# Kernel optimization log

Hardware: AMD Instinct MI355X
Metric: run time of the kernel (lower is better)

Reference implementation:

```python
import jax, jax.numpy as jnp
import numpy as np

D_MODEL = 1024
NUM_HEADS = 16
HEAD_DIM = D_MODEL // NUM_HEADS


def setup_inputs() -> dict:
    key = jax.random.key(0)
    ks = jax.random.split(key, 9)
    s = 1.0 / np.sqrt(D_MODEL)  # torch Linear default init range scale
    def lin(k):
        kw, kb = jax.random.split(k)
        W = jax.random.uniform(kw, (D_MODEL, D_MODEL), jnp.float32, -s, s)
        b = jax.random.uniform(kb, (D_MODEL,), jnp.float32, -s, s)
        return W, b
    Wq, bq = lin(ks[0])
    Wk, bk = lin(ks[1])
    Wv, bv = lin(ks[2])
    Wo, bo = lin(ks[3])
    x = jax.random.normal(ks[4], (4, 2048, D_MODEL), jnp.float32)
    return {"x": x, "Wq": Wq, "bq": bq, "Wk": Wk, "bk": bk,
            "Wv": Wv, "bv": bv, "Wo": Wo, "bo": bo}


def reference(x, Wq, bq, Wk, bk, Wv, bv, Wo, bo):
    B, S, _ = x.shape
    H, Dh = NUM_HEADS, HEAD_DIM
    scale = Dh ** -0.5
    # projections; W stored as [in, out] so y = x @ W + b
    q = (x @ Wq + bq).reshape(B, S, H, Dh).transpose(0, 2, 1, 3)  # [B,H,S,Dh]
    k = (x @ Wk + bk).reshape(B, S, H, Dh).transpose(0, 2, 1, 3)
    v = (x @ Wv + bv).reshape(B, S, H, Dh).transpose(0, 2, 1, 3)
    scores = jnp.einsum('bhqd,bhkd->bhqk', q, k) * scale  # [B,H,S,S]
    causal = jnp.tril(jnp.ones((S, S), dtype=bool))
    scores = jnp.where(causal[None, None], scores, jnp.finfo(scores.dtype).min)
    attn = jax.nn.softmax(scores, axis=-1)
    out = jnp.einsum('bhqk,bhkd->bhqd', attn, v)  # [B,H,S,Dh]
    out = out.transpose(0, 2, 1, 3).reshape(B, S, H * Dh)
    return out @ Wo + bo
```

## Files before the change

kernel.cpp:

```cpp
#include <hip/hip_runtime.h>
#include <math.h>

#define DM 1024
#define NH 16
#define DH 64
#define BB 4
#define SS 2048
#define MROWS (BB*SS)

typedef __bf16 bf16;
typedef __bf16 bf16x8 __attribute__((ext_vector_type(8)));
typedef float floatx4 __attribute__((ext_vector_type(4)));

#if __has_builtin(__builtin_amdgcn_exp2f)
#define EXP2F __builtin_amdgcn_exp2f
#else
#define EXP2F exp2f
#endif

#define QSCALE (0.125f * 1.44269504088896f)

__device__ __forceinline__ void cp16(void* lds, const void* g) {
  __builtin_amdgcn_global_load_lds(
      (__attribute__((address_space(1))) void*)(void*)g,
      (__attribute__((address_space(3))) void*)lds,
      16, 0, 0);
}

__global__ __launch_bounds__(256) void cvt_x(
    const float* __restrict__ X, bf16* __restrict__ Y) {
  int i = (blockIdx.x * 256 + threadIdx.x) * 8;
  float4 a = *(const float4*)&X[i];
  float4 b = *(const float4*)&X[i + 4];
  bf16x8 o;
  o[0] = (bf16)a.x; o[1] = (bf16)a.y; o[2] = (bf16)a.z; o[3] = (bf16)a.w;
  o[4] = (bf16)b.x; o[5] = (bf16)b.y; o[6] = (bf16)b.z; o[7] = (bf16)b.w;
  *(bf16x8*)&Y[i] = o;
}

__global__ __launch_bounds__(1024) void wtransc(
    const float* __restrict__ W0, const float* __restrict__ W1,
    const float* __restrict__ W2, const float* __restrict__ W3,
    bf16* __restrict__ T0, bf16* __restrict__ T1,
    bf16* __restrict__ T2, bf16* __restrict__ T3) {
  __shared__ float tile[32][33];
  const float* W; bf16* T;
  int z = blockIdx.z;
  if (z == 0)      { W = W0; T = T0; }
  else if (z == 1) { W = W1; T = T1; }
  else if (z == 2) { W = W2; T = T2; }
  else             { W = W3; T = T3; }
  int tx = threadIdx.x, ty = threadIdx.y;
  tile[ty][tx] = W[(blockIdx.y * 32 + ty) * DM + blockIdx.x * 32 + tx];
  __syncthreads();
  T[(blockIdx.x * 32 + ty) * DM + blockIdx.y * 32 + tx] = (bf16)tile[tx][ty];
}

#define BK 32
#define TST 136

__global__ __launch_bounds__(256, 3) void gemm_qkv(
    const bf16* __restrict__ A, const bf16* __restrict__ WT,
    const float* __restrict__ bq, const float* __restrict__ bk,
    const float* __restrict__ bv,
    bf16* __restrict__ qb, bf16* __restrict__ kb, bf16* __restrict__ vt) {
  __shared__ __align__(16) char smem[2 * 128 * BK * 2 * 2 > 128 * TST * 2
                                         ? 2 * 128 * BK * 2 * 2
                                         : 128 * TST * 2];
  bf16* As = (bf16*)smem;
  bf16* Bs = (bf16*)smem + 2 * 128 * BK;
  bf16* Ts = (bf16*)smem;

  int tid = threadIdx.x;
  int lane = tid & 63, w = tid >> 6;
  int wm = (w >> 1) * 64;
  int wn = (w & 1) * 64;
  int m0 = blockIdx.y * 128;
  int n0 = blockIdx.x * 128;
  int which = n0 >> 10;
  int qd = lane >> 4;
  int l15 = lane & 15;

  floatx4 acc[4][4] = {};

  auto stage = [&](int pb, int k0) {
    for (int i = 0; i < 2; ++i) {
      int ci = (w * 2 + i) * 64;
      int c = ci + lane;
      int r = c >> 2, cc = (c & 3) * 8;
      cp16(&As[pb * 128 * BK + ci * 8], &A[(size_t)(m0 + r) * DM + k0 + cc]);
      cp16(&Bs[pb * 128 * BK + ci * 8], &WT[(size_t)(n0 + r) * DM + k0 + cc]);
    }
  };

  stage(0, 0);
  __syncthreads();

  for (int t = 0; t < DM / BK; ++t) {
    int pb = t & 1;
    if (t + 1 < DM / BK) stage(pb ^ 1, (t + 1) * BK);
    bf16x8 af[4], bfr[4];
    for (int mt = 0; mt < 4; ++mt)
      af[mt] = *(const bf16x8*)&As[pb * 128 * BK + (wm + mt * 16 + l15) * BK + qd * 8];
    for (int nt = 0; nt < 4; ++nt)
      bfr[nt] = *(const bf16x8*)&Bs[pb * 128 * BK + (wn + nt * 16 + l15) * BK + qd * 8];
    for (int mt = 0; mt < 4; ++mt)
      for (int nt = 0; nt < 4; ++nt)
        acc[mt][nt] = __builtin_amdgcn_mfma_f32_16x16x32_bf16(
            af[mt], bfr[nt], acc[mt][nt], 0, 0, 0);
    __syncthreads();
  }

  const float* bias = (which == 0) ? bq : (which == 1) ? bk : bv;

  if (which == 2) {
    for (int nt = 0; nt < 4; ++nt) {
      int cl = wn + nt * 16 + l15;
      float bv_ = bias[(n0 & 1023) + cl];
      for (int mt = 0; mt < 4; ++mt)
        for (int r = 0; r < 4; ++r)
          Ts[cl * TST + wm + mt * 16 + qd * 4 + r] = (bf16)(acc[mt][nt][r] + bv_);
    }
    __syncthreads();
    int chunk = tid & 15, colb = tid >> 4;
    for (int p = 0; p < 8; ++p) {
      int cl = p * 16 + colb;
      bf16x8 vv = *(const bf16x8*)&Ts[cl * TST + chunk * 8];
      *(bf16x8*)&vt[(size_t)((n0 & 1023) + cl) * MROWS + m0 + chunk * 8] = vv;
    }
  } else {
    bf16* out = (which == 0) ? qb : kb;
    float sc = (which == 0) ? QSCALE : 1.0f;
    for (int nt = 0; nt < 4; ++nt) {
      int col = (n0 & 1023) + wn + nt * 16 + l15;
      float bv_ = bias[col];
      for (int mt = 0; mt < 4; ++mt)
        for (int r = 0; r < 4; ++r) {
          int row = m0 + wm + mt * 16 + qd * 4 + r;
          out[(size_t)row * DM + col] = (bf16)((acc[mt][nt][r] + bv_) * sc);
        }
    }
  }
}

__global__ __launch_bounds__(256, 4) void gemm_out(
    const bf16* __restrict__ A, const bf16* __restrict__ WT,
    const float* __restrict__ bias, float* __restrict__ C) {
  __shared__ __align__(16) bf16 As[2][64 * BK];
  __shared__ __align__(16) bf16 Bs[2][128 * BK];
  int tid = threadIdx.x;
  int lane = tid & 63, w = tid >> 6;
  int wm = (w >> 1) * 32;
  int wn = (w & 1) * 64;
  int m0 = blockIdx.x * 64;
  int n0 = blockIdx.y * 128;
  int qd = lane >> 4;
  int l15 = lane & 15;

  floatx4 acc[2][4] = {};

  auto stage = [&](int pb, int k0) {
    {
      int ci = w * 64;
      int c = ci + lane;
      int r = c >> 2, cc = (c & 3) * 8;
      cp16(&As[pb][ci * 8], &A[(size_t)(m0 + r) * DM + k0 + cc]);
    }
    for (int i = 0; i < 2; ++i) {
      int ci = (w * 2 + i) * 64;
      int c = ci + lane;
      int r = c >> 2, cc = (c & 3) * 8;
      cp16(&Bs[pb][ci * 8], &WT[(size_t)(n0 + r) * DM + k0 + cc]);
    }
  };

  stage(0, 0);
  __syncthreads();

  for (int t = 0; t < DM / BK; ++t) {
    int pb = t & 1;
    if (t + 1 < DM / BK) stage(pb ^ 1, (t + 1) * BK);
    bf16x8 af[2], bfr[4];
    for (int mt = 0; mt < 2; ++mt)
      af[mt] = *(const bf16x8*)&As[pb][(wm + mt * 16 + l15) * BK + qd * 8];
    for (int nt = 0; nt < 4; ++nt)
      bfr[nt] = *(const bf16x8*)&Bs[pb][(wn + nt * 16 + l15) * BK + qd * 8];
    for (int mt = 0; mt < 2; ++mt)
      for (int nt = 0; nt < 4; ++nt)
        acc[mt][nt] = __builtin_amdgcn_mfma_f32_16x16x32_bf16(
            af[mt], bfr[nt], acc[mt][nt], 0, 0, 0);
    __syncthreads();
  }

  for (int nt = 0; nt < 4; ++nt) {
    int col = n0 + wn + nt * 16 + l15;
    float bv = bias[col];
    for (int mt = 0; mt < 2; ++mt)
      for (int r = 0; r < 4; ++r) {
        int row = m0 + wm + mt * 16 + qd * 4 + r;
        C[(size_t)row * DM + col] = acc[mt][nt][r] + bv;
      }
  }
}

__global__ __launch_bounds__(512, 4) void attn_fwd(
    const bf16* __restrict__ Qg, const bf16* __restrict__ Kg,
    const bf16* __restrict__ Vt, bf16* __restrict__ O) {
  __shared__ __align__(16) bf16 Kbuf[2][64 * 64];
  __shared__ __align__(16) bf16 Vbuf[2][64 * 64];
  __shared__ __align__(16) bf16 Ps[8][16][72];

  int tid = threadIdx.x;
  int lane = tid & 63, w = tid >> 6;
  int qd = lane >> 4, l15 = lane & 15;
  int sw = l15 & 7;
  int pair = blockIdx.x, h = blockIdx.y, b = blockIdx.z;
  int base = b * SS;
  int hoff = h * DH;

  int gch = ((lane & 7) ^ (lane >> 3)) * 8;
  auto stage = [&](int pb, int kt) {
    int kbase = base + kt * 64;
    int ci = w * 64;
    int row = (ci + lane) >> 3;
    cp16(&Kbuf[pb][ci * 8], &Kg[(size_t)(kbase + row) * DM + hoff + gch]);
    cp16(&Vbuf[pb][ci * 8],
         &Vt[(size_t)(hoff + row) * MROWS + base + kt * 64 + gch]);
  };

  bf16x8 onesf;
  for (int j = 0; j < 8; ++j) onesf[j] = (bf16)1.0f;

  for (int ph = 0; ph < 2; ++ph) {
    int qt = ph ? (15 - pair) : pair;
    int q0 = qt * 128;
    int nkt = 2 * qt + 2;

    stage(0, 0);

    bf16x8 qf[2];
    {
      int qrow = base + q0 + w * 16 + l15;
      for (int ks = 0; ks < 2; ++ks)
        qf[ks] = *(const bf16x8*)&Qg[(size_t)qrow * DM + hoff + ks * 32 + qd * 8];
    }

    float m_r = -3e38f;
    floatx4 lacc = {};
    floatx4 oacc[4] = {};

    __syncthreads();

    for (int kt = 0; kt < nkt; ++kt) {
      int pb = kt & 1;
      if (kt + 1 < nkt) stage(pb ^ 1, kt + 1);

      floatx4 s[4] = {};
      for (int ks = 0; ks < 2; ++ks)
        for (int nt = 0; nt < 4; ++nt) {
          bf16x8 kf = *(const bf16x8*)
              &Kbuf[pb][(nt * 16 + l15) * 64 + (((ks << 2) + qd) ^ sw) * 8];
          s[nt] = __builtin_amdgcn_mfma_f32_16x16x32_bf16(
              qf[ks], kf, s[nt], 0, 0, 0);
        }

      if (kt >= 2 * qt) {
        for (int nt = 0; nt < 4; ++nt) {
          int col = kt * 64 + nt * 16 + l15;
          for (int r = 0; r < 4; ++r) {
            int row = q0 + w * 16 + qd * 4 + r;
            if (col > row) s[nt][r] = -3e38f;
          }
        }
      }

      {
        float t = s[0][0];
        for (int nt = 0; nt < 4; ++nt)
          for (int r = 0; r < 4; ++r) t = fmaxf(t, s[nt][r]);
        t = fmaxf(t, __shfl_xor(t, 1, 64));
        t = fmaxf(t, __shfl_xor(t, 2, 64));
        t = fmaxf(t, __shfl_xor(t, 4, 64));
        t = fmaxf(t, __shfl_xor(t, 8, 64));
        float mn = fmaxf(m_r, t);
        float al = EXP2F(m_r - mn);
        m_r = mn;
        for (int dt = 0; dt < 4; ++dt)
          for (int r = 0; r < 4; ++r) oacc[dt][r] *= al;
        for (int r = 0; r < 4; ++r) lacc[r] *= al;
        for (int nt = 0; nt < 4; ++nt)
          for (int r = 0; r < 4; ++r) {
            float p = EXP2F(s[nt][r] - mn);
            Ps[w][qd * 4 + r][nt * 16 + l15] = (bf16)p;
          }
      }

      bf16x8 pf[2];
      for (int ks = 0; ks < 2; ++ks)
        pf[ks] = *(const bf16x8*)&Ps[w][l15][ks * 32 + qd * 8];

      for (int ks = 0; ks < 2; ++ks)
        for (int dt = 0; dt < 4; ++dt) {
          bf16x8 vf = *(const bf16x8*)
              &Vbuf[pb][(dt * 16 + l15) * 64 + (((ks << 2) + qd) ^ sw) * 8];
          oacc[dt] = __builtin_amdgcn_mfma_f32_16x16x32_bf16(
              pf[ks], vf, oacc[dt], 0, 0, 0);
        }
      for (int ks = 0; ks < 2; ++ks)
        lacc = __builtin_amdgcn_mfma_f32_16x16x32_bf16(
            pf[ks], onesf, lacc, 0, 0, 0);

      __syncthreads();
    }

    for (int r = 0; r < 4; ++r) {
      float inv = 1.0f / lacc[r];
      int row = base + q0 + w * 16 + qd * 4 + r;
      for (int dt = 0; dt < 4; ++dt)
        O[(size_t)row * DM + hoff + dt * 16 + l15] = (bf16)(oacc[dt][r] * inv);
    }
  }
}

extern "C" void kernel_launch(void* const* d_in, const int* in_sizes, int n_in,
                              void* d_out, int out_size, void* d_ws, size_t ws_size,
                              hipStream_t stream) {
  const float* x  = (const float*)d_in[0];
  const float* Wq = (const float*)d_in[1];
  const float* bq = (const float*)d_in[2];
  const float* Wk = (const float*)d_in[3];
  const float* bk = (const float*)d_in[4];
  const float* Wv = (const float*)d_in[5];
  const float* bv = (const float*)d_in[6];
  const float* Wo = (const float*)d_in[7];
  const float* bo = (const float*)d_in[8];
  float* out = (float*)d_out;

  char* ws = (char*)d_ws;
  const size_t act = (size_t)MROWS * DM * sizeof(bf16);
  bf16* xb    = (bf16*)(ws);
  bf16* qb    = (bf16*)(ws + act);
  bf16* kb    = (bf16*)(ws + 2 * act);
  bf16* vt    = (bf16*)(ws + 3 * act);
  bf16* ab    = (bf16*)(ws + 4 * act);
  bf16* WqkvT = (bf16*)(ws + 5 * act);
  bf16* WoT   = WqkvT + 3 * (size_t)DM * DM;

  cvt_x<<<MROWS * DM / (256 * 8), 256, 0, stream>>>(x, xb);
  wtransc<<<dim3(32, 32, 4), dim3(32, 32), 0, stream>>>(
      Wq, Wk, Wv, Wo,
      WqkvT, WqkvT + (size_t)DM * DM, WqkvT + 2 * (size_t)DM * DM, WoT);

  gemm_qkv<<<dim3(24, 64), 256, 0, stream>>>(
      xb, WqkvT, bq, bk, bv, qb, kb, vt);

  attn_fwd<<<dim3(8, NH, BB), 512, 0, stream>>>(qb, kb, vt, ab);

  gemm_out<<<dim3(128, 8), 256, 0, stream>>>(ab, WoT, bo, out);
}
```

Measured before the change: 268.3 us.

## Keep attention probabilities in registers via transposed QK and permlane swaps

The QK^T MFMA now runs with swapped operands, so each lane holds scores for a single query row. Probabilities are packed to bf16 and rearranged into the PV operand layout with permlane32/16 swaps, which removes the LDS round trip through the Ps buffer. Row sums are accumulated in registers instead of through an extra MFMA against a ones vector. The online softmax also skips rescaling when the new max stays within a threshold of the running max, which cuts exp and multiply work but lets unnormalized values grow by up to 2^11.

```diff
diff --git a/kernel.cpp b/kernel.cpp
--- a/kernel.cpp
+++ b/kernel.cpp
@@ -9,8 +9,11 @@
 #define MROWS (BB*SS)
 
 typedef __bf16 bf16;
+typedef __bf16 bf16x2 __attribute__((ext_vector_type(2)));
 typedef __bf16 bf16x8 __attribute__((ext_vector_type(8)));
 typedef float floatx4 __attribute__((ext_vector_type(4)));
+typedef unsigned int uintx4 __attribute__((ext_vector_type(4)));
+typedef unsigned int uintx2 __attribute__((ext_vector_type(2)));
 
 #if __has_builtin(__builtin_amdgcn_exp2f)
 #define EXP2F __builtin_amdgcn_exp2f
@@ -26,6 +29,32 @@
       (__attribute__((address_space(3))) void*)lds,
       16, 0, 0);
 }
+
+__device__ __forceinline__ unsigned pk2(float a, float b) {
+  bf16x2 t;
+  t[0] = (bf16)a;
+  t[1] = (bf16)b;
+  return __builtin_bit_cast(unsigned, t);
+}
+
+#if __has_builtin(__builtin_amdgcn_permlane32_swap) && \
+    __has_builtin(__builtin_amdgcn_permlane16_swap)
+__device__ __forceinline__ void pl32(unsigned& a, unsigned& b) {
+  uintx2 r = __builtin_amdgcn_permlane32_swap(a, b, false, false);
+  a = r[0]; b = r[1];
+}
+__device__ __forceinline__ void pl16(unsigned& a, unsigned& b) {
+  uintx2 r = __builtin_amdgcn_permlane16_swap(a, b, false, false);
+  a = r[0]; b = r[1];
+}
+#else
+__device__ __forceinline__ void pl32(unsigned& a, unsigned& b) {
+  asm volatile("v_permlane32_swap_b32 %0, %1" : "+v"(a), "+v"(b));
+}
+__device__ __forceinline__ void pl16(unsigned& a, unsigned& b) {
+  asm volatile("v_permlane16_swap_b32 %0, %1" : "+v"(a), "+v"(b));
+}
+#endif
 
 __global__ __launch_bounds__(256) void cvt_x(
     const float* __restrict__ X, bf16* __restrict__ Y) {
@@ -208,7 +237,6 @@
     const bf16* __restrict__ Vt, bf16* __restrict__ O) {
   __shared__ __align__(16) bf16 Kbuf[2][64 * 64];
   __shared__ __align__(16) bf16 Vbuf[2][64 * 64];
-  __shared__ __align__(16) bf16 Ps[8][16][72];
 
   int tid = threadIdx.x;
   int lane = tid & 63, w = tid >> 6;
@@ -228,9 +256,6 @@
          &Vt[(size_t)(hoff + row) * MROWS + base + kt * 64 + gch]);
   };
 
-  bf16x8 onesf;
-  for (int j = 0; j < 8; ++j) onesf[j] = (bf16)1.0f;
-
   for (int ph = 0; ph < 2; ++ph) {
     int qt = ph ? (15 - pair) : pair;
     int q0 = qt * 128;
@@ -246,7 +271,7 @@
     }
 
     float m_r = -3e38f;
-    floatx4 lacc = {};
+    float lacc = 0.0f;
     floatx4 oacc[4] = {};
 
     __syncthreads();
@@ -261,43 +286,51 @@
           bf16x8 kf = *(const bf16x8*)
               &Kbuf[pb][(nt * 16 + l15) * 64 + (((ks << 2) + qd) ^ sw) * 8];
           s[nt] = __builtin_amdgcn_mfma_f32_16x16x32_bf16(
-              qf[ks], kf, s[nt], 0, 0, 0);
+              kf, qf[ks], s[nt], 0, 0, 0);
         }
 
+      int rowq = q0 + w * 16 + l15;
       if (kt >= 2 * qt) {
-        for (int nt = 0; nt < 4; ++nt) {
-          int col = kt * 64 + nt * 16 + l15;
+        for (int nt = 0; nt < 4; ++nt)
           for (int r = 0; r < 4; ++r) {
-            int row = q0 + w * 16 + qd * 4 + r;
-            if (col > row) s[nt][r] = -3e38f;
+            int col = kt * 64 + nt * 16 + qd * 4 + r;
+            if (col > rowq) s[nt][r] = -3e38f;
           }
-        }
       }
 
-      {
-        float t = s[0][0];
-        for (int nt = 0; nt < 4; ++nt)
-          for (int r = 0; r < 4; ++r) t = fmaxf(t, s[nt][r]);
-        t = fmaxf(t, __shfl_xor(t, 1, 64));
-        t = fmaxf(t, __shfl_xor(t, 2, 64));
-        t = fmaxf(t, __shfl_xor(t, 4, 64));
-        t = fmaxf(t, __shfl_xor(t, 8, 64));
+      floatx4 m4 = s[0];
+      for (int nt = 1; nt < 4; ++nt)
+        for (int r = 0; r < 4; ++r) m4[r] = fmaxf(m4[r], s[nt][r]);
+      float t = fmaxf(fmaxf(m4[0], m4[1]), fmaxf(m4[2], m4[3]));
+      t = fmaxf(t, __shfl_xor(t, 16, 64));
+      t = fmaxf(t, __shfl_xor(t, 32, 64));
+
+      if (!__all(t <= m_r + 11.0f)) {
         float mn = fmaxf(m_r, t);
         float al = EXP2F(m_r - mn);
         m_r = mn;
         for (int dt = 0; dt < 4; ++dt)
           for (int r = 0; r < 4; ++r) oacc[dt][r] *= al;
-        for (int r = 0; r < 4; ++r) lacc[r] *= al;
-        for (int nt = 0; nt < 4; ++nt)
-          for (int r = 0; r < 4; ++r) {
-            float p = EXP2F(s[nt][r] - mn);
-            Ps[w][qd * 4 + r][nt * 16 + l15] = (bf16)p;
-          }
+        lacc *= al;
       }
 
       bf16x8 pf[2];
-      for (int ks = 0; ks < 2; ++ks)
-        pf[ks] = *(const bf16x8*)&Ps[w][l15][ks * 32 + qd * 8];
+      for (int ks = 0; ks < 2; ++ks) {
+        float pu[4], pv[4];
+        for (int r = 0; r < 4; ++r) {
+          pu[r] = EXP2F(s[2 * ks][r] - m_r);
+          pv[r] = EXP2F(s[2 * ks + 1][r] - m_r);
+        }
+        lacc += ((pu[0] + pu[1]) + (pu[2] + pu[3])) +
+                ((pv[0] + pv[1]) + (pv[2] + pv[3]));
+        unsigned u0 = pk2(pu[0], pu[1]), u1 = pk2(pu[2], pu[3]);
+        unsigned v0 = pk2(pv[0], pv[1]), v1 = pk2(pv[2], pv[3]);
+        pl32(u0, v0); pl16(u0, v0);
+        pl32(u1, v1); pl16(u1, v1);
+        uintx4 ww;
+        ww[0] = u0; ww[1] = u1; ww[2] = v0; ww[3] = v1;
+        pf[ks] = __builtin_bit_cast(bf16x8, ww);
+      }
 
       for (int ks = 0; ks < 2; ++ks)
         for (int dt = 0; dt < 4; ++dt) {
@@ -306,15 +339,14 @@
           oacc[dt] = __builtin_amdgcn_mfma_f32_16x16x32_bf16(
               pf[ks], vf, oacc[dt], 0, 0, 0);
         }
-      for (int ks = 0; ks < 2; ++ks)
-        lacc = __builtin_amdgcn_mfma_f32_16x16x32_bf16(
-            pf[ks], onesf, lacc, 0, 0, 0);
 
       __syncthreads();
     }
 
+    lacc += __shfl_xor(lacc, 16, 64);
+    lacc += __shfl_xor(lacc, 32, 64);
     for (int r = 0; r < 4; ++r) {
-      float inv = 1.0f / lacc[r];
+      float inv = 1.0f / __shfl(lacc, qd * 4 + r, 64);
       int row = base + q0 + w * 16 + qd * 4 + r;
       for (int dt = 0; dt < 4; ++dt)
         O[(size_t)row * DM + hoff + dt * 16 + l15] = (bf16)(oacc[dt][r] * inv);
```

Result: faster. 258.7 us (-3.6%).
